# Performance work log

Measured on AMD Instinct MI355X. Metric: run time of the kernel, lower is better.

The kernel has to match this reference:

```python
import jax, jax.numpy as jnp
import numpy as np

D_MODEL = 1024
NUM_HEADS = 16
D_K = D_MODEL // NUM_HEADS  # 64
B, T = 2, 2048


def rope_tables(seq_len, d_k):
    # Matches RotaryPositionalEmbedding + the slice apply_rotary takes:
    # only cos/sin of freqs (dim d_k//2) are used.
    half = d_k // 2
    inv_freq = 1.0 / (10000.0 ** (jnp.arange(0, d_k, 2, dtype=jnp.float32) / d_k))  # (half,)
    t = jnp.arange(seq_len, dtype=jnp.float32)
    freqs = jnp.einsum('i,j->ij', t, inv_freq)  # (T, half)
    return jnp.cos(freqs), jnp.sin(freqs)


def apply_rotary(x, cos, sin):
    # x: (B, H, T, D); rotate first 2*half dims as two halves
    half = x.shape[-1] // 2
    x1, x2 = x[..., :half], x[..., half:2 * half]
    c = cos[None, None, :x.shape[2], :half]
    s = sin[None, None, :x.shape[2], :half]
    return jnp.concatenate([x1 * c - x2 * s, x1 * s + x2 * c], axis=-1)


def setup_inputs() -> dict:
    key = jax.random.key(0)
    ks = jax.random.split(key, 5)
    scale = 1.0 / np.sqrt(D_MODEL)
    return {
        'x': jax.random.normal(ks[0], (B, T, D_MODEL), dtype=jnp.float32),
        'wq': jax.random.normal(ks[1], (D_MODEL, D_MODEL), dtype=jnp.float32) * scale,
        'wk': jax.random.normal(ks[2], (D_MODEL, D_MODEL), dtype=jnp.float32) * scale,
        'wv': jax.random.normal(ks[3], (D_MODEL, D_MODEL), dtype=jnp.float32) * scale,
        'wo': jax.random.normal(ks[4], (D_MODEL, D_MODEL), dtype=jnp.float32) * scale,
    }


def reference(x, wq, wk, wv, wo):
    Bs, Ts, _ = x.shape
    def proj(w):
        # nn.Linear: x @ w.T, then split heads -> (B, H, T, d_k)
        return (x @ w.T).reshape(Bs, Ts, NUM_HEADS, D_K).transpose(0, 2, 1, 3)
    Q, K, V = proj(wq), proj(wk), proj(wv)
    cos, sin = rope_tables(Ts, D_K)
    Q = apply_rotary(Q, cos, sin)
    K = apply_rotary(K, cos, sin)
    scores = jnp.einsum('bhqd,bhkd->bhqk', Q, K) / jnp.sqrt(jnp.float32(D_K))
    attn = jax.nn.softmax(scores, axis=-1)  # dropout is identity in eval
    out = jnp.einsum('bhqk,bhkd->bhqd', attn, V)
    out = out.transpose(0, 2, 1, 3).reshape(Bs, Ts, D_MODEL)
    return out @ wo.T
```

## Files before the change

kernel.cpp:

```cpp
#include <hip/hip_runtime.h>
#include <math.h>

typedef __attribute__((ext_vector_type(8))) short short8;
typedef __attribute__((ext_vector_type(4))) short short4v;
typedef __attribute__((ext_vector_type(4))) float f32x4;
typedef __attribute__((ext_vector_type(16))) float f32x16;

#define D_MODEL 1024
#define NUM_HEADS 16
#define D_K 64
#define B_SZ 2
#define T_SZ 2048
#define M_ROWS (B_SZ * T_SZ)
#define LSTR 72
#define LOG2E 1.4426950408889634f
#define KVSPLIT 1024

__device__ __forceinline__ unsigned short f2bf(float f) {
    union { float f; unsigned int u; } v; v.f = f;
    unsigned int r = v.u + 0x7FFF + ((v.u >> 16) & 1);
    return (unsigned short)(r >> 16);
}
__device__ __forceinline__ void gload_lds16(const void* g, void* l) {
    __builtin_amdgcn_global_load_lds(
        (const __attribute__((address_space(1))) unsigned int*)g,
        (__attribute__((address_space(3))) unsigned int*)l, 16, 0, 0);
}
__device__ __forceinline__ int cvtpk(float lo, float hi) {
    int r;
    asm("v_cvt_pk_bf16_f32 %0, %1, %2" : "=v"(r) : "v"(lo), "v"(hi));
    return r;
}
__device__ __forceinline__ float fast_exp2(float x) {
#if __has_builtin(__builtin_amdgcn_exp2f)
    return __builtin_amdgcn_exp2f(x);
#else
    float r; asm("v_exp_f32 %0, %1" : "=v"(r) : "v"(x)); return r;
#endif
}

__global__ __launch_bounds__(256) void cvt_all(
    const float* __restrict__ x,  const float* __restrict__ w0,
    const float* __restrict__ w1, const float* __restrict__ w2,
    const float* __restrict__ w3, unsigned short* __restrict__ dst)
{
    const size_t NX8 = (size_t)M_ROWS * D_MODEL / 8;
    const size_t NW8 = (size_t)D_MODEL * D_MODEL / 8;
    size_t i = (size_t)blockIdx.x * 256 + threadIdx.x;
    const float* src; size_t off;
    if (i < NX8) { src = x; off = i; }
    else {
        size_t j = i - NX8;
        int ws = (int)(j >> 17);
        off = j & (NW8 - 1);
        src = (ws == 0) ? w0 : (ws == 1) ? w1 : (ws == 2) ? w2 : w3;
    }
    const float4* p = (const float4*)src + 2 * off;
    float4 a = p[0], b = p[1];
    short8 o;
    o[0] = f2bf(a.x); o[1] = f2bf(a.y); o[2] = f2bf(a.z); o[3] = f2bf(a.w);
    o[4] = f2bf(b.x); o[5] = f2bf(b.y); o[6] = f2bf(b.z); o[7] = f2bf(b.w);
    *((short8*)dst + i) = o;
}

__global__ __launch_bounds__(256) void rope_table(float2* __restrict__ tab)
{
    int idx = blockIdx.x * 256 + threadIdx.x;
    int t = idx >> 5, i = idx & 31;
    const float invf = (float)pow(10000.0, -(double)i / 32.0);
    float s, c;
    sincosf((float)t * invf, &s, &c);
    tab[idx] = make_float2(c, s);
}

__global__ __launch_bounds__(256) void gemm_qkv(
    const unsigned short* __restrict__ Xb,
    const unsigned short* __restrict__ Wb,
    unsigned short* __restrict__ Qb,
    unsigned short* __restrict__ Kb,
    unsigned short* __restrict__ Vtg,
    const float2* __restrict__ tab)
{
    __shared__ unsigned short Als[128 * 64];
    __shared__ unsigned short Bls[128 * 64];

    const int tid = threadIdx.x;
    const int lane = tid & 63, wid = tid >> 6;
    const int g = lane >> 4, c16 = lane & 15;
    const int wr = wid >> 1, wc = wid & 1;

    const int bid = blockIdx.x;
    const int swz = (bid & 7) * 96 + (bid >> 3);
    const int bm = swz / 24, bn = swz % 24;
    const int m0 = bm * 128, n0p = bn * 128;
    const int z = n0p >> 10, n0c = n0p & 1023;

    const int l8 = lane >> 3, l7 = lane & 7;
    const int scol = 8 * (l7 ^ l8);
    const unsigned short* xsrc = Xb + (size_t)(m0 + wid * 32 + l8) * D_MODEL + scol;
    const unsigned short* wsrc = Wb + (size_t)(n0p + wid * 32 + l8) * D_MODEL + scol;

    f32x4 acc[4][4] = {};

    for (int k0 = 0; k0 < D_MODEL; k0 += 64) {
        __syncthreads();
#pragma unroll
        for (int i = 0; i < 4; i++) {
            gload_lds16(xsrc + (size_t)i * 8 * D_MODEL + k0, Als + (wid * 32 + i * 8) * 64);
            gload_lds16(wsrc + (size_t)i * 8 * D_MODEL + k0, Bls + (wid * 32 + i * 8) * 64);
        }
        __syncthreads();
#pragma unroll
        for (int kk = 0; kk < 64; kk += 32) {
            short8 af[4], bf[4];
            const int sw = (c16 & 7) * 8;
#pragma unroll
            for (int mf = 0; mf < 4; mf++)
                af[mf] = *(const short8*)&Als[(wr * 64 + mf * 16 + c16) * 64 +
                                              ((kk + g * 8) ^ sw)];
#pragma unroll
            for (int nf = 0; nf < 4; nf++)
                bf[nf] = *(const short8*)&Bls[(wc * 64 + nf * 16 + c16) * 64 +
                                              ((kk + g * 8) ^ sw)];
#pragma unroll
            for (int mf = 0; mf < 4; mf++)
#pragma unroll
                for (int nf = 0; nf < 4; nf++)
                    acc[mf][nf] = __builtin_amdgcn_mfma_f32_16x16x32_bf16(
                        af[mf], bf[nf], acc[mf][nf], 0, 0, 0);
        }
    }

    if (z < 2) {
        const float qs = (z == 0) ? 0.125f * LOG2E : 1.0f;
        unsigned short* Y = (z == 0) ? Qb : Kb;
#pragma unroll
        for (int mf = 0; mf < 4; mf++)
#pragma unroll
            for (int j = 0; j < 4; j++) {
                int row = m0 + wr * 64 + mf * 16 + g * 4 + j;
                int t = row & (T_SZ - 1);
#pragma unroll
                for (int nf = 0; nf < 2; nf++) {
                    float2 cs = tab[t * 32 + nf * 16 + c16];
                    float a = acc[mf][nf][j], b2 = acc[mf][nf + 2][j];
                    acc[mf][nf][j]     = (a * cs.x - b2 * cs.y) * qs;
                    acc[mf][nf + 2][j] = (a * cs.y + b2 * cs.x) * qs;
                }
            }
#pragma unroll
        for (int mf = 0; mf < 4; mf++)
#pragma unroll
            for (int nf = 0; nf < 4; nf++)
#pragma unroll
                for (int j = 0; j < 4; j++) {
                    int row = m0 + wr * 64 + mf * 16 + g * 4 + j;
                    int col = n0c + wc * 64 + nf * 16 + c16;
                    Y[(size_t)row * D_MODEL + col] = f2bf(acc[mf][nf][j]);
                }
    } else {
#pragma unroll
        for (int mf = 0; mf < 4; mf++) {
            int row0 = m0 + wr * 64 + mf * 16 + g * 4;
            int bq = row0 >> 11;
            int t0 = row0 & (T_SZ - 1);
#pragma unroll
            for (int nf = 0; nf < 4; nf++) {
                int col = n0c + wc * 64 + nf * 16 + c16;
                int h = col >> 6, d = col & 63;
                short4v pk;
#pragma unroll
                for (int j = 0; j < 4; j++) pk[j] = (short)f2bf(acc[mf][nf][j]);
                *(short4v*)&Vtg[(size_t)((bq * 16 + h) * 64 + d) * T_SZ + t0] = pk;
            }
        }
    }
}

__global__ __launch_bounds__(256) void gemm_out(
    const unsigned short* __restrict__ Xb,
    const unsigned short* __restrict__ W,
    float* __restrict__ Y)
{
    __shared__ unsigned short Als[128 * 64];
    __shared__ unsigned short Bls[64 * 64];

    const int tid = threadIdx.x;
    const int lane = tid & 63, wid = tid >> 6;
    const int g = lane >> 4, c16 = lane & 15;
    const int wr = wid >> 1, wc = wid & 1;
    const int m0 = blockIdx.y * 128, n0 = blockIdx.x * 64;

    const int l8 = lane >> 3, l7 = lane & 7;
    const int scol = 8 * (l7 ^ l8);
    const unsigned short* xsrc = Xb + (size_t)(m0 + wid * 32 + l8) * D_MODEL + scol;
    const unsigned short* wsrc = W + (size_t)(n0 + wid * 16 + l8) * D_MODEL + scol;

    f32x4 acc[4][2] = {};

    for (int k0 = 0; k0 < D_MODEL; k0 += 64) {
        __syncthreads();
#pragma unroll
        for (int i = 0; i < 4; i++)
            gload_lds16(xsrc + (size_t)i * 8 * D_MODEL + k0, Als + (wid * 32 + i * 8) * 64);
#pragma unroll
        for (int j = 0; j < 2; j++)
            gload_lds16(wsrc + (size_t)j * 8 * D_MODEL + k0, Bls + (wid * 16 + j * 8) * 64);
        __syncthreads();
#pragma unroll
        for (int kk = 0; kk < 64; kk += 32) {
            short8 af[4], bf[2];
            const int sw = (c16 & 7) * 8;
#pragma unroll
            for (int mf = 0; mf < 4; mf++)
                af[mf] = *(const short8*)&Als[(wr * 64 + mf * 16 + c16) * 64 +
                                              ((kk + g * 8) ^ sw)];
#pragma unroll
            for (int nf = 0; nf < 2; nf++)
                bf[nf] = *(const short8*)&Bls[(wc * 32 + nf * 16 + c16) * 64 +
                                              ((kk + g * 8) ^ sw)];
#pragma unroll
            for (int mf = 0; mf < 4; mf++)
#pragma unroll
                for (int nf = 0; nf < 2; nf++)
                    acc[mf][nf] = __builtin_amdgcn_mfma_f32_16x16x32_bf16(
                        af[mf], bf[nf], acc[mf][nf], 0, 0, 0);
        }
    }

#pragma unroll
    for (int mf = 0; mf < 4; mf++)
#pragma unroll
        for (int nf = 0; nf < 2; nf++)
#pragma unroll
            for (int j = 0; j < 4; j++) {
                int row = m0 + wr * 64 + mf * 16 + g * 4 + j;
                int col = n0 + wc * 32 + nf * 16 + c16;
                Y[(size_t)row * D_MODEL + col] = acc[mf][nf][j];
            }
}

#define PVAL(i) ((i) < 16 ? s0[(i) & 15] : s1[(i) & 15])

__global__ __launch_bounds__(512, 4) void attn_mfma32(
    const unsigned short* __restrict__ Qb,
    const unsigned short* __restrict__ Kb,
    const unsigned short* __restrict__ Vtg,
    unsigned short* __restrict__ Ob)
{
    __shared__ __align__(16) char smem[36864];

    const int tid = threadIdx.x;
    const int lane = tid & 63, wid = tid >> 6;
    const int kz = wid >> 2, wq = wid & 3;
    const int q32 = lane & 31, hi = lane >> 5;
    const int bh = blockIdx.y, b = bh >> 4, h = bh & (NUM_HEADS - 1);
    const int q0 = blockIdx.x * 128 + wq * 32;

    unsigned short* Ks = (unsigned short*)(smem + kz * 18432);
    unsigned short* Vt = Ks + 64 * LSTR;

    short8 qf[4];
    {
        const unsigned short* qsrc =
            Qb + (size_t)(b * T_SZ + q0 + q32) * D_MODEL + h * D_K + 8 * hi;
#pragma unroll
        for (int s = 0; s < 4; s++) qf[s] = *(const short8*)(qsrc + 16 * s);
    }

    f32x16 oacc0 = {}, oacc1 = {};
    float l = 0.f;

    const int t256 = tid & 255;
    const int krow = t256 >> 2, kcb = t256 & 3;
    const unsigned short* kbase =
        Kb + (size_t)(b * T_SZ + kz * KVSPLIT) * D_MODEL + h * D_K;
    const unsigned short* vtbase =
        Vtg + (size_t)((b * 16 + h) * 64) * T_SZ + kz * KVSPLIT;

    short8 pk0, pk1, pv0, pv1;
#define LOAD_KV(KT) do { \
    const unsigned short* _s = kbase + (size_t)((KT) + krow) * D_MODEL + kcb * 16; \
    pk0 = *(const short8*)_s; pk1 = *(const short8*)(_s + 8); \
    const unsigned short* _v = vtbase + (size_t)krow * T_SZ + (KT) + kcb * 16; \
    pv0 = *(const short8*)_v; pv1 = *(const short8*)(_v + 8); \
  } while (0)

    LOAD_KV(0);

    for (int kt = 0; kt < KVSPLIT; kt += 64) {
        __builtin_amdgcn_sched_barrier(0);
        __builtin_amdgcn_s_barrier();
        __builtin_amdgcn_sched_barrier(0);
        *(short8*)&Ks[krow * LSTR + kcb * 16] = pk0;
        *(short8*)&Ks[krow * LSTR + kcb * 16 + 8] = pk1;
        *(short8*)&Vt[krow * LSTR + kcb * 16] = pv0;
        *(short8*)&Vt[krow * LSTR + kcb * 16 + 8] = pv1;
        if (kt + 64 < KVSPLIT) LOAD_KV(kt + 64);
        asm volatile("s_waitcnt lgkmcnt(0)" ::: "memory");
        __builtin_amdgcn_s_barrier();
        __builtin_amdgcn_sched_barrier(0);

        f32x16 s0 = {}, s1 = {};
        __builtin_amdgcn_s_setprio(1);
#pragma unroll
        for (int s = 0; s < 4; s++) {
            short8 ak0 = *(const short8*)&Ks[q32 * LSTR + 16 * s + 8 * hi];
            short8 ak1 = *(const short8*)&Ks[(32 + q32) * LSTR + 16 * s + 8 * hi];
            s0 = __builtin_amdgcn_mfma_f32_32x32x16_bf16(ak0, qf[s], s0, 0, 0, 0);
            s1 = __builtin_amdgcn_mfma_f32_32x32x16_bf16(ak1, qf[s], s1, 0, 0, 0);
        }
        __builtin_amdgcn_s_setprio(0);

        float ps = 0.f;
#pragma unroll
        for (int r = 0; r < 16; r++) s0[r] = fast_exp2(s0[r]);
#pragma unroll
        for (int r = 0; r < 16; r++) s1[r] = fast_exp2(s1[r]);
#pragma unroll
        for (int r = 0; r < 16; r++) ps += s0[r] + s1[r];
        l += ps;

        __builtin_amdgcn_s_setprio(1);
#pragma unroll
        for (int t = 0; t < 4; t++) {
            const int b0 = 4 * ((2 * t + 0) & 3) + 16 * (t >> 1);
            const int b1 = 4 * ((2 * t + 1) & 3) + 16 * (t >> 1);
            int X0 = cvtpk(PVAL(b0), PVAL(b0 + 1));
            int X1 = cvtpk(PVAL(b0 + 2), PVAL(b0 + 3));
            int Y0 = cvtpk(PVAL(b1), PVAL(b1 + 1));
            int Y1 = cvtpk(PVAL(b1 + 2), PVAL(b1 + 3));
            asm("v_permlane32_swap_b32 %0, %1" : "+v"(X0), "+v"(Y0));
            asm("v_permlane32_swap_b32 %0, %1" : "+v"(X1), "+v"(Y1));
            union { int w[4]; short8 v; } af;
            af.w[0] = X0; af.w[1] = X1; af.w[2] = Y0; af.w[3] = Y1;
            short8 bv0 = *(const short8*)&Vt[q32 * LSTR + 16 * t + 8 * hi];
            short8 bv1 = *(const short8*)&Vt[(32 + q32) * LSTR + 16 * t + 8 * hi];
            oacc0 = __builtin_amdgcn_mfma_f32_32x32x16_bf16(af.v, bv0, oacc0, 0, 0, 0);
            oacc1 = __builtin_amdgcn_mfma_f32_32x32x16_bf16(af.v, bv1, oacc1, 0, 0, 0);
        }
        __builtin_amdgcn_s_setprio(0);
    }

    l += __shfl_xor(l, 32);

    __syncthreads();
    float* cmbO = (float*)smem;
    float* lb   = (float*)(smem + 32768);
    if (kz == 1) {
        if (hi == 0) lb[wq * 32 + q32] = l;
#pragma unroll
        for (int r = 0; r < 16; r++) {
            int qr = (r & 3) + 8 * (r >> 2) + 4 * hi;
            cmbO[wq * 2048 + qr * 64 + q32]      = oacc0[r];
            cmbO[wq * 2048 + qr * 64 + 32 + q32] = oacc1[r];
        }
    }
    __syncthreads();
    if (kz == 0) {
        float linv = 1.f / (l + lb[wq * 32 + q32]);
#pragma unroll
        for (int r = 0; r < 16; r++) {
            int qr = (r & 3) + 8 * (r >> 2) + 4 * hi;
            float iv = __shfl(linv, qr);
            float o0 = (oacc0[r] + cmbO[wq * 2048 + qr * 64 + q32]) * iv;
            float o1 = (oacc1[r] + cmbO[wq * 2048 + qr * 64 + 32 + q32]) * iv;
            size_t row = (size_t)(b * T_SZ + q0 + qr);
            Ob[row * D_MODEL + h * D_K + q32]      = f2bf(o0);
            Ob[row * D_MODEL + h * D_K + 32 + q32] = f2bf(o1);
        }
    }
}

extern "C" void kernel_launch(void* const* d_in, const int* in_sizes, int n_in,
                              void* d_out, int out_size, void* d_ws, size_t ws_size,
                              hipStream_t stream)
{
    const float* x  = (const float*)d_in[0];
    const float* wq = (const float*)d_in[1];
    const float* wk = (const float*)d_in[2];
    const float* wv = (const float*)d_in[3];
    const float* wo = (const float*)d_in[4];
    float* out = (float*)d_out;

    const size_t NX = (size_t)M_ROWS * D_MODEL;
    const size_t NW = (size_t)D_MODEL * D_MODEL;
    unsigned short* xb  = (unsigned short*)d_ws;
    unsigned short* wqb = xb + NX;
    unsigned short* wkb = wqb + NW;
    unsigned short* wvb = wkb + NW;
    unsigned short* wob = wvb + NW;
    unsigned short* Qb  = wob + NW;
    unsigned short* Kb  = Qb + NX;
    unsigned short* Vtg = Kb + NX;
    unsigned short* Ob  = Vtg + NX;
    float2* tab = (float2*)(Ob + NX);

    const int ncvt8 = (int)((NX + 4 * NW) / 8);
    cvt_all<<<dim3(ncvt8 / 256), dim3(256), 0, stream>>>(x, wq, wk, wv, wo, xb);
    rope_table<<<dim3(T_SZ * 32 / 256), dim3(256), 0, stream>>>(tab);

    gemm_qkv<<<dim3(768), dim3(256), 0, stream>>>(xb, wqb, Qb, Kb, Vtg, tab);

    attn_mfma32<<<dim3(T_SZ / 128, B_SZ * NUM_HEADS), dim3(512), 0, stream>>>(
        Qb, Kb, Vtg, Ob);

    gemm_out<<<dim3(D_MODEL / 64, M_ROWS / 128), dim3(256), 0, stream>>>(Ob, wob, out);
}
```

Measured before the change: 190.4 us.

## Remap block indices for XCD-local L2 reuse and fuse prep kernels

Block-to-tile mappings in the QKV GEMM, attention and output GEMM are remapped so that blocks dispatched round-robin to the same XCD share input tiles (rows of X or W, or the same attention head's K/V). The aim is better per-XCD L2 hit rates and less HBM/infinity-fabric traffic. The rope-table kernel is also merged into the conversion kernel as extra blocks, removing one launch. The mapping assumes blocks are dispatched across 8 XCDs by blockIdx modulo 8 and assumes the exact grid sizes used here.

New measurement: 180.6 us. 1.05x faster.

```diff
diff --git a/kernel.cpp b/kernel.cpp
--- a/kernel.cpp
+++ b/kernel.cpp
@@ -39,13 +39,23 @@
 #endif
 }
 
-__global__ __launch_bounds__(256) void cvt_all(
+__global__ __launch_bounds__(256) void prep_all(
     const float* __restrict__ x,  const float* __restrict__ w0,
     const float* __restrict__ w1, const float* __restrict__ w2,
-    const float* __restrict__ w3, unsigned short* __restrict__ dst)
+    const float* __restrict__ w3, unsigned short* __restrict__ dst,
+    float2* __restrict__ tab)
 {
     const size_t NX8 = (size_t)M_ROWS * D_MODEL / 8;
     const size_t NW8 = (size_t)D_MODEL * D_MODEL / 8;
+    if (blockIdx.x >= 4096) {
+        int idx = (blockIdx.x - 4096) * 256 + threadIdx.x;
+        int t = idx >> 5, i = idx & 31;
+        const float invf = (float)pow(10000.0, -(double)i / 32.0);
+        float s, c;
+        sincosf((float)t * invf, &s, &c);
+        tab[idx] = make_float2(c, s);
+        return;
+    }
     size_t i = (size_t)blockIdx.x * 256 + threadIdx.x;
     const float* src; size_t off;
     if (i < NX8) { src = x; off = i; }
@@ -61,16 +71,6 @@
     o[0] = f2bf(a.x); o[1] = f2bf(a.y); o[2] = f2bf(a.z); o[3] = f2bf(a.w);
     o[4] = f2bf(b.x); o[5] = f2bf(b.y); o[6] = f2bf(b.z); o[7] = f2bf(b.w);
     *((short8*)dst + i) = o;
-}
-
-__global__ __launch_bounds__(256) void rope_table(float2* __restrict__ tab)
-{
-    int idx = blockIdx.x * 256 + threadIdx.x;
-    int t = idx >> 5, i = idx & 31;
-    const float invf = (float)pow(10000.0, -(double)i / 32.0);
-    float s, c;
-    sincosf((float)t * invf, &s, &c);
-    tab[idx] = make_float2(c, s);
 }
 
 __global__ __launch_bounds__(256) void gemm_qkv(
@@ -90,8 +90,9 @@
     const int wr = wid >> 1, wc = wid & 1;
 
     const int bid = blockIdx.x;
-    const int swz = (bid & 7) * 96 + (bid >> 3);
-    const int bm = swz / 24, bn = swz % 24;
+    const int xcd = bid & 7, slot = bid >> 3;
+    const int bm = (xcd & 3) * 8 + (slot & 7);
+    const int bn = (xcd >> 2) * 12 + (slot >> 3);
     const int m0 = bm * 128, n0p = bn * 128;
     const int z = n0p >> 10, n0c = n0p & 1023;
 
@@ -189,7 +190,12 @@
     const int lane = tid & 63, wid = tid >> 6;
     const int g = lane >> 4, c16 = lane & 15;
     const int wr = wid >> 1, wc = wid & 1;
-    const int m0 = blockIdx.y * 128, n0 = blockIdx.x * 64;
+
+    const int bid = blockIdx.x;
+    const int xcd = bid & 7, slot = bid >> 3;
+    const int bm = (xcd & 3) * 8 + (slot & 7);
+    const int bn = (xcd >> 2) * 8 + (slot >> 3);
+    const int m0 = bm * 128, n0 = bn * 64;
 
     const int l8 = lane >> 3, l7 = lane & 7;
     const int scol = 8 * (l7 ^ l8);
@@ -254,8 +260,13 @@
     const int lane = tid & 63, wid = tid >> 6;
     const int kz = wid >> 2, wq = wid & 3;
     const int q32 = lane & 31, hi = lane >> 5;
-    const int bh = blockIdx.y, b = bh >> 4, h = bh & (NUM_HEADS - 1);
-    const int q0 = blockIdx.x * 128 + wq * 32;
+
+    const int raw = blockIdx.x;
+    const int xcd = raw & 7, slot = raw >> 3;
+    const int bh = xcd * 4 + (slot >> 4);
+    const int qblk = slot & 15;
+    const int b = bh >> 4, h = bh & (NUM_HEADS - 1);
+    const int q0 = qblk * 128 + wq * 32;
 
     unsigned short* Ks = (unsigned short*)(smem + kz * 18432);
     unsigned short* Vt = Ks + 64 * LSTR;
@@ -396,14 +407,11 @@
     unsigned short* Ob  = Vtg + NX;
     float2* tab = (float2*)(Ob + NX);
 
-    const int ncvt8 = (int)((NX + 4 * NW) / 8);
-    cvt_all<<<dim3(ncvt8 / 256), dim3(256), 0, stream>>>(x, wq, wk, wv, wo, xb);
-    rope_table<<<dim3(T_SZ * 32 / 256), dim3(256), 0, stream>>>(tab);
+    prep_all<<<dim3(4096 + 256), dim3(256), 0, stream>>>(x, wq, wk, wv, wo, xb, tab);
 
     gemm_qkv<<<dim3(768), dim3(256), 0, stream>>>(xb, wqb, Qb, Kb, Vtg, tab);
 
-    attn_mfma32<<<dim3(T_SZ / 128, B_SZ * NUM_HEADS), dim3(512), 0, stream>>>(
-        Qb, Kb, Vtg, Ob);
-
-    gemm_out<<<dim3(D_MODEL / 64, M_ROWS / 128), dim3(256), 0, stream>>>(Ob, wob, out);
-}
+    attn_mfma32<<<dim3(512), dim3(512), 0, stream>>>(Qb, Kb, Vtg, Ob);
+
+    gemm_out<<<dim3(512), dim3(256), 0, stream>>>(Ob, wob, out);
+}
```
